# Optimization experiments

Hardware: AMD Instinct MI355X
Metric: run time of the kernel (lower is better)

The kernel has to match this reference:

```python
import jax, jax.numpy as jnp
import numpy as np

NUM_CLASSES = 5
TOPK = 10
ALPHA = 0.5
BETA = 6.0
TEMPERATURE = 2.0
EPS = 1e-9
RADIUS = 1.5
MAXF = 5  # max fallback anchors per tiny GT


def setup_inputs() -> dict:
    key = jax.random.key(0)
    ks = jax.random.split(key, 6)
    B, A, G, C = 16, 8400, 128, NUM_CLASSES
    pred_scores = jax.random.normal(ks[0], (B, A, C), jnp.float32)
    pred_bboxes = jax.random.uniform(ks[1], (B, A, 5), jnp.float32)
    anchor_points = jax.random.uniform(ks[2], (A, 2), jnp.float32)
    gt_labels = jax.random.randint(ks[3], (B, G, 1), 0, C, jnp.int32)
    gt_bboxes = jax.random.uniform(ks[4], (B, G, 5), jnp.float32)
    mask_gt = jax.random.randint(ks[5], (B, G, 1), 0, 2, jnp.int32)
    return dict(pred_scores=pred_scores, pred_bboxes=pred_bboxes,
                anchor_points=anchor_points, gt_labels=gt_labels,
                gt_bboxes=gt_bboxes, mask_gt=mask_gt)


def reference(pred_scores, pred_bboxes, anchor_points, gt_labels, gt_bboxes, mask_gt):
    B, A, C = pred_scores.shape
    G = gt_bboxes.shape[1]
    labels = gt_labels[..., 0].astype(jnp.int32)          # [B,G]
    mask = mask_gt[..., 0] > 0                            # [B,G]

    # ---- get_box_metrics ----
    cls_scores = jnp.clip(jax.nn.sigmoid(pred_scores), EPS, 1.0)            # [B,A,C]
    bbox_scores = jnp.take_along_axis(
        cls_scores, jnp.broadcast_to(labels[:, None, :], (B, A, G)), axis=2)  # [B,A,G]
    pred_cxcy = pred_bboxes[:, :, None, :2]                                  # [B,A,1,2]
    gt_cxcy = gt_bboxes[:, None, :, :2]                                      # [B,1,G,2]
    distances = jnp.linalg.norm(pred_cxcy - gt_cxcy, axis=-1)                # [B,A,G]
    gt_wh = gt_bboxes[:, None, :, 2:4]                                       # [B,1,G,2]
    scale = jnp.sqrt(gt_wh[..., 0] * gt_wh[..., 1])                          # [B,1,G]
    overlaps = jnp.exp(-(distances / (scale + 1e-6)) ** 2)                   # [B,A,G]
    align_metric = jnp.exp(ALPHA * jnp.log(bbox_scores + EPS)
                           + BETA * jnp.log(overlaps + EPS))
    ap = anchor_points.reshape(1, A, 1, 2)
    center_dist = jnp.linalg.norm(ap - gt_cxcy, axis=-1)                     # [B,A,G]
    center_weight = jnp.exp(-(center_dist / (scale * 1.5 + 1e-6)) ** 2)
    align_metric = align_metric * center_weight

    # ---- select_candidates_in_gts (rotated boxes) ----
    theta = gt_bboxes[:, None, :, 4]                                         # [B,1,G]
    dx = ap[..., 0] - gt_cxcy[..., 0]
    dy = ap[..., 1] - gt_cxcy[..., 1]
    cos_t, sin_t = jnp.cos(-theta), jnp.sin(-theta)
    local_dx = dx * cos_t - dy * sin_t
    local_dy = dx * sin_t + dy * cos_t
    is_in = ((jnp.abs(local_dx) < gt_wh[..., 0] * RADIUS)
             & (jnp.abs(local_dy) < gt_wh[..., 1] * RADIUS))                 # [B,A,G]

    # ---- tiny-object fallback (unconditional, gated by tiny_missed mask;
    #      equivalent to torch's data-dependent `if` branch) ----
    gt_area = gt_bboxes[..., 2] * gt_bboxes[..., 3]                          # [B,G]
    cand_per_gt = is_in.sum(axis=1)                                          # [B,G]
    tiny_missed = mask & (gt_area < 0.01) & (cand_per_gt == 0)
    fallback_k = jnp.where(gt_area < 0.002, 5, 3)                            # [B,G]
    dist_ga = jnp.linalg.norm(
        gt_bboxes[:, :, None, :2] - anchor_points[None, None, :, :], axis=-1)  # [B,G,A]
    _, closest_idx = jax.lax.top_k(-dist_ga, MAXF)                           # [B,G,5]
    seq = jnp.arange(MAXF)[None, None, :]
    valid_fb = tiny_missed[:, :, None] & (seq < fallback_k[:, :, None])      # [B,G,5]
    b_grid = jnp.arange(B)[:, None, None]
    g_grid = jnp.arange(G)[None, :, None]
    fb = jnp.zeros((B, A, G), jnp.int32).at[b_grid, closest_idx, g_grid].max(
        valid_fb.astype(jnp.int32))
    is_in = is_in | (fb > 0)

    align_metric = align_metric * is_in.astype(align_metric.dtype)

    # ---- select_topk_candidates ----
    am_gT = jnp.swapaxes(align_metric, 1, 2) * mask[:, :, None].astype(align_metric.dtype)  # [B,G,A]
    ov_gT = jnp.swapaxes(overlaps, 1, 2)                                     # [B,G,A]
    topk_metrics, topk_idxs = jax.lax.top_k(am_gT, TOPK)                     # [B,G,K]
    topk_overlaps = jnp.take_along_axis(ov_gT, topk_idxs, axis=2)
    dynamic_k = jnp.clip(jnp.round(topk_overlaps.sum(-1)), 1.0, float(TOPK)) # [B,G]
    k_mask = jnp.arange(TOPK)[None, None, :] < dynamic_k[:, :, None]
    pos_vals = (topk_metrics > EPS) & k_mask
    is_pos_gT = jnp.zeros((B, G, A), bool).at[b_grid, g_grid, topk_idxs].set(pos_vals)

    align_metric = jnp.swapaxes(am_gT, 1, 2)                                 # [B,A,G] (GT-masked)
    is_pos = jnp.swapaxes(is_pos_gT, 1, 2)                                   # [B,A,G]
    anchor_to_gt = jnp.argmax(align_metric, axis=-1)                         # [B,A]
    is_pos_mask = is_pos.sum(-1) > 0                                         # [B,A]
    target_labels = jnp.take_along_axis(labels, anchor_to_gt, axis=1)        # [B,A]
    target_bboxes = jnp.take_along_axis(
        gt_bboxes, jnp.broadcast_to(anchor_to_gt[:, :, None], (B, A, 5)), axis=1)  # [B,A,5]
    am_max = align_metric.max(axis=1, keepdims=True)                         # [B,1,G]
    norm_am = align_metric / (am_max + EPS) * overlaps                       # [B,A,G]
    raw = jnp.take_along_axis(norm_am, anchor_to_gt[:, :, None], axis=2)[..., 0]  # [B,A]
    valid = (target_labels >= 0) & (target_labels < C) & is_pos_mask
    raw_safe = jnp.where(raw > 0, raw, 1.0)
    soft = jnp.where(raw > 0, raw_safe ** (1.0 / TEMPERATURE), 0.0)
    target_scores = jax.nn.one_hot(target_labels, C, dtype=pred_scores.dtype) \
        * (soft * valid.astype(soft.dtype))[..., None]                       # [B,A,C]
    return target_labels, target_bboxes, target_scores, is_pos_mask
```

## Files before the change

### kernel.cpp

```cpp
#include <hip/hip_runtime.h>
#include <math.h>

#define NB 16
#define NA 8400
#define NG 128
#define NC 5
#define KTOP 10
#define MAXF 5


__global__ __launch_bounds__(256) void k_logsig(
    const float* __restrict__ pred_scores, double* __restrict__ table, int n)
{
    int i = blockIdx.x * 256 + threadIdx.x;
    if (i < n) {
        double x = (double)pred_scores[i];
        double s = 1.0 / (1.0 + exp(-x));
        s = fmin(fmax(s, 1e-9), 1.0);
        table[i] = log(s + 1e-9);
    }
}


__global__ __launch_bounds__(256) void k_assign(
    const float* __restrict__ pred_bboxes,
    const float* __restrict__ anchor_points,
    const int*   __restrict__ gt_labels,
    const float* __restrict__ gt_bboxes,
    const int*   __restrict__ mask_gt,
    const double* __restrict__ logsig,
    int* __restrict__ fb_cnt,
    int* __restrict__ fb_idx,
    double* __restrict__ am_max,
    int* __restrict__ pos_mask)
{
    int bg = blockIdx.x;
    int b = bg / NG;
    int tid = threadIdx.x;

    const float* gbb = gt_bboxes + (size_t)bg * 5;
    double cx = gbb[0], cy = gbb[1], w = gbb[2], h = gbb[3], th = gbb[4];
    double ct = cos(-th), st = sin(-th);
    int m = mask_gt[bg];
    double area = (double)gbb[2] * (double)gbb[3];

    __shared__ double Sv[KTOP][256];
    __shared__ int    Si[KTOP][256];
    __shared__ double rv[256];
    __shared__ int    ri[256];
    __shared__ double wv_s[KTOP];
    __shared__ int    wi_s[KTOP];
    __shared__ int    s_icnt[256];
    __shared__ int    s_win[MAXF];
    __shared__ int    s_k;

    bool need_fb = (m > 0) && (area < 0.01);
    if (tid == 0) s_k = 0;
    if (need_fb) {
        int cnt = 0;
        double ld[MAXF]; int li[MAXF];
#pragma unroll
        for (int t = 0; t < MAXF; t++) { ld[t] = 1e300; li[t] = 0x7fffffff; }
        for (int a = tid; a < NA; a += 256) {
            double ax = anchor_points[a * 2], ay = anchor_points[a * 2 + 1];
            double cdx = ax - cx, cdy = ay - cy;
            double ldx = cdx * ct - cdy * st;
            double ldy = cdx * st + cdy * ct;
            if (fabs(ldx) < w * 1.5 && fabs(ldy) < h * 1.5) cnt++;
            double d = sqrt(cdx * cdx + cdy * cdy);
            double cv = d; int ci = a;
#pragma unroll
            for (int p = 0; p < MAXF; p++) {
                bool better = (cv < ld[p]) || (cv == ld[p] && ci < li[p]);
                double tv = ld[p]; int ti = li[p];
                if (better) { ld[p] = cv; li[p] = ci; cv = tv; ci = ti; }
            }
        }
        s_icnt[tid] = cnt;
#pragma unroll
        for (int t = 0; t < MAXF; t++) { Sv[t][tid] = ld[t]; Si[t][tid] = li[t]; }
        __syncthreads();
        for (int s2 = 128; s2 > 0; s2 >>= 1) {
            if (tid < s2) s_icnt[tid] += s_icnt[tid + s2];
            __syncthreads();
        }
        int ptr = 0;
        for (int j = 0; j < MAXF; j++) {
            double hv = (ptr < MAXF) ? Sv[ptr][tid] : 1e300;
            int    hi = (ptr < MAXF) ? Si[ptr][tid] : 0x7fffffff;
            rv[tid] = hv; ri[tid] = hi;
            __syncthreads();
            for (int s2 = 128; s2 > 0; s2 >>= 1) {
                if (tid < s2) {
                    bool better = (rv[tid + s2] < rv[tid]) ||
                                  (rv[tid + s2] == rv[tid] && ri[tid + s2] < ri[tid]);
                    if (better) { rv[tid] = rv[tid + s2]; ri[tid] = ri[tid + s2]; }
                }
                __syncthreads();
            }
            int Wi = ri[0];
            if (tid == 0) s_win[j] = Wi;
            __syncthreads();
            if (ptr < MAXF && hi == Wi) ptr++;
        }
        if (tid == 0) {
            int total = s_icnt[0];
            int k = 0;
            if (total == 0) k = (area < 0.002) ? 5 : 3;
            s_k = k;
            for (int j = 0; j < MAXF; j++) fb_idx[bg * MAXF + j] = s_win[j];
        }
        __syncthreads();
    }
    if (tid == 0) fb_cnt[bg] = s_k;

    if (m <= 0) {
        if (tid == 0) am_max[bg] = 0.0;
        return;
    }
    __syncthreads();

    double scale = sqrt(w * h);
    int lbl = gt_labels[bg];
    int fcnt = s_k;
    int fidx[MAXF];
#pragma unroll
    for (int t = 0; t < MAXF; t++) fidx[t] = need_fb ? s_win[t] : 0x7fffffff;

    double lv[KTOP]; int li2[KTOP];
#pragma unroll
    for (int t = 0; t < KTOP; t++) { lv[t] = -1.0; li2[t] = 0x7fffffff; }

    for (int a = tid; a < NA; a += 256) {
        double ax = anchor_points[a * 2], ay = anchor_points[a * 2 + 1];
        double cdx = ax - cx, cdy = ay - cy;
        double ldx = cdx * ct - cdy * st;
        double ldy = cdx * st + cdy * ct;
        bool inb = (fabs(ldx) < w * 1.5) && (fabs(ldy) < h * 1.5);
        bool fb = false;
#pragma unroll
        for (int t = 0; t < MAXF; t++) if (t < fcnt && fidx[t] == a) fb = true;
        double amm = 0.0;
        if (inb || fb) {
            double lgs = logsig[((size_t)b * NA + a) * NC + lbl];
            double px = pred_bboxes[((size_t)b * NA + a) * 5 + 0];
            double py = pred_bboxes[((size_t)b * NA + a) * 5 + 1];
            double dx = px - cx, dy = py - cy;
            double d  = sqrt(dx * dx + dy * dy);
            double r  = d / (scale + 1e-6);
            double e1 = exp(-(r * r));
            double L  = log(e1 + 1e-9);
            double cd = sqrt(cdx * cdx + cdy * cdy);
            double cr = cd / (scale * 1.5 + 1e-6);
            amm = exp(0.5 * lgs + 6.0 * L - cr * cr);
        }
        double cv = amm; int ci = a;
#pragma unroll
        for (int p = 0; p < KTOP; p++) {
            bool better = (cv > lv[p]) || (cv == lv[p] && ci < li2[p]);
            double tv = lv[p]; int ti = li2[p];
            if (better) { lv[p] = cv; li2[p] = ci; cv = tv; ci = ti; }
        }
    }

#pragma unroll
    for (int t = 0; t < KTOP; t++) { Sv[t][tid] = lv[t]; Si[t][tid] = li2[t]; }
    __syncthreads();

    int ptr = 0;
    for (int j = 0; j < KTOP; j++) {
        double hv = (ptr < KTOP) ? Sv[ptr][tid] : -1.0;
        int    hi = (ptr < KTOP) ? Si[ptr][tid] : 0x7fffffff;
        rv[tid] = hv; ri[tid] = hi;
        __syncthreads();
        for (int s2 = 128; s2 > 0; s2 >>= 1) {
            if (tid < s2) {
                bool better = (rv[tid + s2] > rv[tid]) ||
                              (rv[tid + s2] == rv[tid] && ri[tid + s2] < ri[tid]);
                if (better) { rv[tid] = rv[tid + s2]; ri[tid] = ri[tid + s2]; }
            }
            __syncthreads();
        }
        int Wi = ri[0];
        if (tid == 0) { wv_s[j] = rv[0]; wi_s[j] = Wi; }
        __syncthreads();
        if (ptr < KTOP && hi == Wi) ptr++;
    }

    if (tid == 0) {
        am_max[bg] = wv_s[0];
        double ssum = 0.0;
        for (int j = 0; j < KTOP; j++) {
            int aW = wi_s[j];
            double px = pred_bboxes[((size_t)b * NA + aW) * 5 + 0];
            double py = pred_bboxes[((size_t)b * NA + aW) * 5 + 1];
            double dx = px - cx, dy = py - cy;
            double d = sqrt(dx * dx + dy * dy);
            double r = d / (scale + 1e-6);
            ssum += exp(-(r * r));
        }
        double rk = rint(ssum);
        rk = fmin(fmax(rk, 1.0), 10.0);
        for (int j = 0; j < KTOP; j++) {
            if (wv_s[j] > 1e-9 && (double)j < rk)
                atomicOr(&pos_mask[b * NA + wi_s[j]], 1);
        }
    }
}


__global__ __launch_bounds__(256) void k_final(
    const float* __restrict__ pred_bboxes,
    const float* __restrict__ anchor_points,
    const int*   __restrict__ gt_labels,
    const float* __restrict__ gt_bboxes,
    const int*   __restrict__ mask_gt,
    const double* __restrict__ logsig,
    const int*   __restrict__ fb_cnt,
    const int*   __restrict__ fb_idx,
    const double* __restrict__ am_max,
    const int*   __restrict__ pos_mask,
    float* __restrict__ out)
{
    __shared__ double s_cx[NG], s_cy[NG], s_ct[NG], s_st[NG], s_scale[NG], s_w[NG], s_h[NG], s_am[NG];
    __shared__ int s_lbl[NG], s_msk[NG], s_fcnt[NG];
    __shared__ int s_fidx[NG][MAXF];
    __shared__ double mv[4][64];
    __shared__ int    mg[4][64];
    __shared__ double mo[4][64];

    int b = blockIdx.y;
    int tid = threadIdx.x;
    if (tid < NG) {
        int g = tid, bg = b * NG + g;
        const float* gbb = gt_bboxes + (size_t)bg * 5;
        double th = gbb[4];
        s_cx[g] = gbb[0]; s_cy[g] = gbb[1]; s_w[g] = gbb[2]; s_h[g] = gbb[3];
        s_ct[g] = cos(-th); s_st[g] = sin(-th);
        s_scale[g] = sqrt((double)gbb[2] * (double)gbb[3]);
        s_am[g] = am_max[bg];
        s_lbl[g] = gt_labels[bg];
        s_msk[g] = mask_gt[bg];
        s_fcnt[g] = fb_cnt[bg];
        for (int t = 0; t < MAXF; t++) s_fidx[g][t] = fb_idx[bg * MAXF + t];
    }
    __syncthreads();

    int al = tid & 63;
    int slice = tid >> 6;
    int a = blockIdx.x * 64 + al;

    double best = -1.0; int bestg = slice * 32; double bov = 0.0;
    if (a < NA) {
        double px = pred_bboxes[((size_t)b * NA + a) * 5 + 0];
        double py = pred_bboxes[((size_t)b * NA + a) * 5 + 1];
        double ax = anchor_points[a * 2], ay = anchor_points[a * 2 + 1];
        const double* lg = logsig + ((size_t)b * NA + a) * NC;
        double l0 = lg[0], l1 = lg[1], l2 = lg[2], l3 = lg[3], l4 = lg[4];

        int g0 = slice * 32;
        for (int g = g0; g < g0 + 32; g++) {
            int lbl = s_lbl[g];
            double lgs = (lbl == 0) ? l0 : (lbl == 1) ? l1 : (lbl == 2) ? l2 : (lbl == 3) ? l3 : l4;
            bool fb = false;
            int fc = s_fcnt[g];
#pragma unroll
            for (int t = 0; t < MAXF; t++) if (t < fc && s_fidx[g][t] == a) fb = true;
            double cdx = ax - s_cx[g], cdy = ay - s_cy[g];
            double ldx = cdx * s_ct[g] - cdy * s_st[g];
            double ldy = cdx * s_st[g] + cdy * s_ct[g];
            bool inb = (fabs(ldx) < s_w[g] * 1.5) && (fabs(ldy) < s_h[g] * 1.5);
            double amm = 0.0, e1 = 0.0;
            if ((inb || fb) && s_msk[g] > 0) {
                double dx = px - s_cx[g], dy = py - s_cy[g];
                double d = sqrt(dx * dx + dy * dy);
                double r = d / (s_scale[g] + 1e-6);
                e1 = exp(-(r * r));
                double L = log(e1 + 1e-9);
                double cd = sqrt(cdx * cdx + cdy * cdy);
                double cr = cd / (s_scale[g] * 1.5 + 1e-6);
                amm = exp(0.5 * lgs + 6.0 * L - cr * cr);
            }
            if (amm > best) { best = amm; bestg = g; bov = e1; }
        }
    }

    mv[slice][al] = best; mg[slice][al] = bestg; mo[slice][al] = bov;
    __syncthreads();

    if (tid < 64) {
        int a2 = blockIdx.x * 64 + tid;
        if (a2 < NA) {
            double B = mv[0][tid]; int G = mg[0][tid]; double OV = mo[0][tid];
#pragma unroll
            for (int s = 1; s < 4; s++) {
                if (mv[s][tid] > B) { B = mv[s][tid]; G = mg[s][tid]; OV = mo[s][tid]; }
            }
            int lbl = s_lbl[G];
            bool pos = pos_mask[b * NA + a2] != 0;
            bool valid = (lbl >= 0 && lbl < NC) && pos;
            double raw = B / (s_am[G] + 1e-9) * OV;
            double soft = (raw > 0.0) ? sqrt(raw) : 0.0;

            size_t ba = (size_t)b * NA + a2;
            out[ba] = (float)lbl;
            const float* gb2 = gt_bboxes + ((size_t)b * NG + G) * 5;
            float* ob = out + (size_t)NB * NA + ba * 5;
            ob[0] = gb2[0]; ob[1] = gb2[1]; ob[2] = gb2[2]; ob[3] = gb2[3]; ob[4] = gb2[4];
            float* os = out + (size_t)NB * NA * 6 + ba * 5;
            float sval = valid ? (float)soft : 0.0f;
#pragma unroll
            for (int c = 0; c < NC; c++) os[c] = (c == lbl) ? sval : 0.0f;
            out[(size_t)NB * NA * 11 + ba] = pos ? 1.0f : 0.0f;
        }
    }
}


extern "C" void kernel_launch(void* const* d_in, const int* in_sizes, int n_in,
                              void* d_out, int out_size, void* d_ws, size_t ws_size,
                              hipStream_t stream)
{
    const float* pred_scores   = (const float*)d_in[0];
    const float* pred_bboxes   = (const float*)d_in[1];
    const float* anchor_points = (const float*)d_in[2];
    const int*   gt_labels     = (const int*)d_in[3];
    const float* gt_bboxes     = (const float*)d_in[4];
    const int*   mask_gt       = (const int*)d_in[5];
    float* out = (float*)d_out;

    char* ws = (char*)d_ws;
    size_t off = 0;
    int* pos_mask = (int*)(ws + off);
    off += (size_t)NB * NA * sizeof(int);
    off = (off + 255) & ~(size_t)255;
    double* amax = (double*)(ws + off);
    off += (size_t)NB * NG * sizeof(double);
    off = (off + 255) & ~(size_t)255;
    int* fb_cnt = (int*)(ws + off);
    off += (size_t)NB * NG * sizeof(int);
    off = (off + 255) & ~(size_t)255;
    int* fb_idx = (int*)(ws + off);
    off += (size_t)NB * NG * MAXF * sizeof(int);
    off = (off + 255) & ~(size_t)255;
    double* logsig = (double*)(ws + off);

    hipMemsetAsync(pos_mask, 0, (size_t)NB * NA * sizeof(int), stream);

    int nls = NB * NA * NC;
    k_logsig<<<(nls + 255) / 256, 256, 0, stream>>>(pred_scores, logsig, nls);
    k_assign<<<NB * NG, 256, 0, stream>>>(pred_bboxes, anchor_points, gt_labels,
                                          gt_bboxes, mask_gt, logsig,
                                          fb_cnt, fb_idx, amax, pos_mask);
    k_final<<<dim3((NA + 63) / 64, NB), 256, 0, stream>>>(
        pred_bboxes, anchor_points, gt_labels, gt_bboxes, mask_gt, logsig,
        fb_cnt, fb_idx, amax, pos_mask, out);
}
```

Baseline: 337.2 us.

## Add float upper-bound pruning before fp64 metric, wavefront top-k merges, fuse memset

Replaces the fp64 log-sigmoid table with a float table and adds a cheap float upper bound on the alignment metric. In both k_assign and k_final, the exact double-precision computation runs only when that bound could beat the current threshold: a shared atomicMax bar in k_assign, the running best in k_final. The block-wide shared-memory top-k reductions become wavefront shuffle reductions followed by a 4-way serial merge, and zeroing pos_mask is folded into the prep kernel instead of a separate memset. The safety margin on the float bound has to cover the fast-math error so results stay exact, and the extra branching adds divergence.

```diff
diff --git a/kernel.cpp b/kernel.cpp
--- a/kernel.cpp
+++ b/kernel.cpp
@@ -8,27 +8,35 @@
 #define KTOP 10
 #define MAXF 5
 
-
-__global__ __launch_bounds__(256) void k_logsig(
-    const float* __restrict__ pred_scores, double* __restrict__ table, int n)
+static __device__ __forceinline__ double lgs64_of(float x) {
+    double s = 1.0 / (1.0 + exp(-(double)x));
+    s = fmin(fmax(s, 1e-9), 1.0);
+    return log(s + 1e-9);
+}
+
+
+__global__ __launch_bounds__(256) void k_prep(
+    const float* __restrict__ ps, float* __restrict__ tab, int* __restrict__ pos_mask)
 {
     int i = blockIdx.x * 256 + threadIdx.x;
-    if (i < n) {
-        double x = (double)pred_scores[i];
-        double s = 1.0 / (1.0 + exp(-x));
-        s = fmin(fmax(s, 1e-9), 1.0);
-        table[i] = log(s + 1e-9);
-    }
+    if (i < NB * NA * NC) {
+        float x = ps[i];
+        float s = 1.0f / (1.0f + __expf(-x));
+        s = fminf(fmaxf(s, 1e-9f), 1.0f);
+        tab[i] = __logf(s + 1e-9f);
+    }
+    if (i < NB * NA) pos_mask[i] = 0;
 }
 
 
 __global__ __launch_bounds__(256) void k_assign(
+    const float* __restrict__ pred_scores,
     const float* __restrict__ pred_bboxes,
     const float* __restrict__ anchor_points,
     const int*   __restrict__ gt_labels,
     const float* __restrict__ gt_bboxes,
     const int*   __restrict__ mask_gt,
-    const double* __restrict__ logsig,
+    const float* __restrict__ lg32,
     int* __restrict__ fb_cnt,
     int* __restrict__ fb_idx,
     double* __restrict__ am_max,
@@ -37,74 +45,82 @@
     int bg = blockIdx.x;
     int b = bg / NG;
     int tid = threadIdx.x;
+    int lane = tid & 63;
+    int wid = tid >> 6;
 
     const float* gbb = gt_bboxes + (size_t)bg * 5;
-    double cx = gbb[0], cy = gbb[1], w = gbb[2], h = gbb[3], th = gbb[4];
+    float cxf = gbb[0], cyf = gbb[1];
+    double cx = cxf, cy = cyf, w = gbb[2], h = gbb[3], th = gbb[4];
     double ct = cos(-th), st = sin(-th);
+    double w15 = w * 1.5, h15 = h * 1.5;
     int m = mask_gt[bg];
-    double area = (double)gbb[2] * (double)gbb[3];
-
-    __shared__ double Sv[KTOP][256];
-    __shared__ int    Si[KTOP][256];
-    __shared__ double rv[256];
-    __shared__ int    ri[256];
+    double area = w * h;
+
+    __shared__ unsigned s_bar_u;
+    __shared__ double LwV[4][KTOP];
+    __shared__ int    LwI[4][KTOP];
     __shared__ double wv_s[KTOP];
     __shared__ int    wi_s[KTOP];
-    __shared__ int    s_icnt[256];
     __shared__ int    s_win[MAXF];
     __shared__ int    s_k;
+    __shared__ int    s_cnt;
 
     bool need_fb = (m > 0) && (area < 0.01);
-    if (tid == 0) s_k = 0;
+    if (tid == 0) { s_k = 0; s_cnt = 0; s_bar_u = 0u; }
+    __syncthreads();
+
     if (need_fb) {
         int cnt = 0;
-        double ld[MAXF]; int li[MAXF];
-#pragma unroll
-        for (int t = 0; t < MAXF; t++) { ld[t] = 1e300; li[t] = 0x7fffffff; }
+        double ld[MAXF]; int lid[MAXF];
+#pragma unroll
+        for (int t = 0; t < MAXF; t++) { ld[t] = 1e300; lid[t] = 0x7fffffff; }
         for (int a = tid; a < NA; a += 256) {
-            double ax = anchor_points[a * 2], ay = anchor_points[a * 2 + 1];
-            double cdx = ax - cx, cdy = ay - cy;
+            float axf = anchor_points[2 * a], ayf = anchor_points[2 * a + 1];
+            double cdx = (double)axf - cx, cdy = (double)ayf - cy;
             double ldx = cdx * ct - cdy * st;
             double ldy = cdx * st + cdy * ct;
-            if (fabs(ldx) < w * 1.5 && fabs(ldy) < h * 1.5) cnt++;
+            if (fabs(ldx) < w15 && fabs(ldy) < h15) cnt++;
             double d = sqrt(cdx * cdx + cdy * cdy);
             double cv = d; int ci = a;
 #pragma unroll
             for (int p = 0; p < MAXF; p++) {
-                bool better = (cv < ld[p]) || (cv == ld[p] && ci < li[p]);
-                double tv = ld[p]; int ti = li[p];
-                if (better) { ld[p] = cv; li[p] = ci; cv = tv; ci = ti; }
-            }
-        }
-        s_icnt[tid] = cnt;
-#pragma unroll
-        for (int t = 0; t < MAXF; t++) { Sv[t][tid] = ld[t]; Si[t][tid] = li[t]; }
+                bool better = (cv < ld[p]) || (cv == ld[p] && ci < lid[p]);
+                double tv = ld[p]; int ti = lid[p];
+                if (better) { ld[p] = cv; lid[p] = ci; cv = tv; ci = ti; }
+            }
+        }
+        for (int off = 32; off; off >>= 1) cnt += __shfl_xor(cnt, off);
+        if (lane == 0) atomicAdd(&s_cnt, cnt);
+        for (int j = 0; j < MAXF; j++) {
+            double bv = ld[0]; int bi = lid[0];
+            int hi = lid[0];
+            for (int off = 32; off; off >>= 1) {
+                double ov = __shfl_xor(bv, off); int oi = __shfl_xor(bi, off);
+                if (ov < bv || (ov == bv && oi < bi)) { bv = ov; bi = oi; }
+            }
+            if (lane == 0) { LwV[wid][j] = bv; LwI[wid][j] = bi; }
+            if (hi == bi) {
+#pragma unroll
+                for (int p = 0; p < MAXF - 1; p++) { ld[p] = ld[p + 1]; lid[p] = lid[p + 1]; }
+                ld[MAXF - 1] = 1e301; lid[MAXF - 1] = 0x7fffffff;
+            }
+        }
         __syncthreads();
-        for (int s2 = 128; s2 > 0; s2 >>= 1) {
-            if (tid < s2) s_icnt[tid] += s_icnt[tid + s2];
-            __syncthreads();
-        }
-        int ptr = 0;
-        for (int j = 0; j < MAXF; j++) {
-            double hv = (ptr < MAXF) ? Sv[ptr][tid] : 1e300;
-            int    hi = (ptr < MAXF) ? Si[ptr][tid] : 0x7fffffff;
-            rv[tid] = hv; ri[tid] = hi;
-            __syncthreads();
-            for (int s2 = 128; s2 > 0; s2 >>= 1) {
-                if (tid < s2) {
-                    bool better = (rv[tid + s2] < rv[tid]) ||
-                                  (rv[tid + s2] == rv[tid] && ri[tid + s2] < ri[tid]);
-                    if (better) { rv[tid] = rv[tid + s2]; ri[tid] = ri[tid + s2]; }
-                }
-                __syncthreads();
-            }
-            int Wi = ri[0];
-            if (tid == 0) s_win[j] = Wi;
-            __syncthreads();
-            if (ptr < MAXF && hi == Wi) ptr++;
-        }
         if (tid == 0) {
-            int total = s_icnt[0];
+            int p0 = 0, p1 = 0, p2 = 0, p3 = 0;
+            for (int j = 0; j < MAXF; j++) {
+                double h0 = (p0 < MAXF) ? LwV[0][p0] : 1e302; int i0 = (p0 < MAXF) ? LwI[0][p0] : 0x7fffffff;
+                double h1 = (p1 < MAXF) ? LwV[1][p1] : 1e302; int i1 = (p1 < MAXF) ? LwI[1][p1] : 0x7fffffff;
+                double h2 = (p2 < MAXF) ? LwV[2][p2] : 1e302; int i2 = (p2 < MAXF) ? LwI[2][p2] : 0x7fffffff;
+                double h3 = (p3 < MAXF) ? LwV[3][p3] : 1e302; int i3 = (p3 < MAXF) ? LwI[3][p3] : 0x7fffffff;
+                double bv = h0; int bi = i0; int bw = 0;
+                if (h1 < bv || (h1 == bv && i1 < bi)) { bv = h1; bi = i1; bw = 1; }
+                if (h2 < bv || (h2 == bv && i2 < bi)) { bv = h2; bi = i2; bw = 2; }
+                if (h3 < bv || (h3 == bv && i3 < bi)) { bv = h3; bi = i3; bw = 3; }
+                s_win[j] = bi;
+                if (bw == 0) p0++; else if (bw == 1) p1++; else if (bw == 2) p2++; else p3++;
+            }
+            int total = s_cnt;
             int k = 0;
             if (total == 0) k = (area < 0.002) ? 5 : 3;
             s_k = k;
@@ -121,79 +137,112 @@
     __syncthreads();
 
     double scale = sqrt(w * h);
+    float scalef = (float)scale;
+    float sef = scalef + 1e-6f;
+    float se2f = scalef * 1.5f + 1e-6f;
     int lbl = gt_labels[bg];
     int fcnt = s_k;
     int fidx[MAXF];
 #pragma unroll
     for (int t = 0; t < MAXF; t++) fidx[t] = need_fb ? s_win[t] : 0x7fffffff;
 
-    double lv[KTOP]; int li2[KTOP];
-#pragma unroll
-    for (int t = 0; t < KTOP; t++) { lv[t] = -1.0; li2[t] = 0x7fffffff; }
+    double lv[KTOP]; int li[KTOP];
+#pragma unroll
+    for (int t = 0; t < KTOP; t++) { lv[t] = -1.0; li[t] = 0x7fffffff; }
 
     for (int a = tid; a < NA; a += 256) {
-        double ax = anchor_points[a * 2], ay = anchor_points[a * 2 + 1];
-        double cdx = ax - cx, cdy = ay - cy;
+        float axf = anchor_points[2 * a], ayf = anchor_points[2 * a + 1];
+        double cdx = (double)axf - cx, cdy = (double)ayf - cy;
         double ldx = cdx * ct - cdy * st;
         double ldy = cdx * st + cdy * ct;
-        bool inb = (fabs(ldx) < w * 1.5) && (fabs(ldy) < h * 1.5);
-        bool fb = false;
-#pragma unroll
-        for (int t = 0; t < MAXF; t++) if (t < fcnt && fidx[t] == a) fb = true;
-        double amm = 0.0;
-        if (inb || fb) {
-            double lgs = logsig[((size_t)b * NA + a) * NC + lbl];
-            double px = pred_bboxes[((size_t)b * NA + a) * 5 + 0];
-            double py = pred_bboxes[((size_t)b * NA + a) * 5 + 1];
-            double dx = px - cx, dy = py - cy;
-            double d  = sqrt(dx * dx + dy * dy);
-            double r  = d / (scale + 1e-6);
-            double e1 = exp(-(r * r));
-            double L  = log(e1 + 1e-9);
-            double cd = sqrt(cdx * cdx + cdy * cdy);
-            double cr = cd / (scale * 1.5 + 1e-6);
-            amm = exp(0.5 * lgs + 6.0 * L - cr * cr);
-        }
-        double cv = amm; int ci = a;
-#pragma unroll
-        for (int p = 0; p < KTOP; p++) {
-            bool better = (cv > lv[p]) || (cv == lv[p] && ci < li2[p]);
-            double tv = lv[p]; int ti = li2[p];
-            if (better) { lv[p] = cv; li2[p] = ci; cv = tv; ci = ti; }
-        }
-    }
-
-#pragma unroll
-    for (int t = 0; t < KTOP; t++) { Sv[t][tid] = lv[t]; Si[t][tid] = li2[t]; }
+        bool inb = (fabs(ldx) < w15) && (fabs(ldy) < h15);
+        bool fbh = false;
+#pragma unroll
+        for (int t = 0; t < MAXF; t++) if (t < fcnt && fidx[t] == a) fbh = true;
+        double amm = 0.0; bool have = false;
+        if (inb || fbh) {
+            float pxf = pred_bboxes[((size_t)b * NA + a) * 5 + 0];
+            float pyf = pred_bboxes[((size_t)b * NA + a) * 5 + 1];
+            float lgsf = lg32[((size_t)b * NA + a) * NC + lbl];
+            float dxf = pxf - cxf, dyf = pyf - cyf;
+            float rf = sqrtf(dxf * dxf + dyf * dyf) / sef;
+            float e1f = __expf(-(rf * rf));
+            float Lf = __logf(e1f + 1e-9f);
+            float cdxf = axf - cxf, cdyf = ayf - cyf;
+            float crf = sqrtf(cdxf * cdxf + cdyf * cdyf) / se2f;
+            float t1 = 0.5f * lgsf, t2 = 6.0f * Lf, t3 = crf * crf;
+            float t32 = t1 + t2 - t3;
+            float mm = 2e-4f + 2e-5f * (fabsf(t1) + fabsf(t2) + t3);
+            float ub = __expf(t32 + mm);
+            float barf = __uint_as_float(*(volatile unsigned*)&s_bar_u);
+            if (!(ub < barf)) {
+                double lgs = lgs64_of(pred_scores[((size_t)b * NA + a) * NC + lbl]);
+                double px = (double)pxf, py = (double)pyf;
+                double dx = px - cx, dy = py - cy;
+                double d  = sqrt(dx * dx + dy * dy);
+                double r  = d / (scale + 1e-6);
+                double e1 = exp(-(r * r));
+                double L  = log(e1 + 1e-9);
+                double cd = sqrt(cdx * cdx + cdy * cdy);
+                double cr = cd / (scale * 1.5 + 1e-6);
+                amm = exp(0.5 * lgs + 6.0 * L - cr * cr);
+                have = true;
+            }
+        } else {
+            float barf = __uint_as_float(*(volatile unsigned*)&s_bar_u);
+            if (barf == 0.0f) { amm = 0.0; have = true; }
+        }
+        if (have) {
+            double cv = amm; int ci = a;
+#pragma unroll
+            for (int p = 0; p < KTOP; p++) {
+                bool better = (cv > lv[p]) || (cv == lv[p] && ci < li[p]);
+                double tv = lv[p]; int ti = li[p];
+                if (better) { lv[p] = cv; li[p] = ci; cv = tv; ci = ti; }
+            }
+            if (lv[KTOP - 1] > 0.0) {
+                unsigned nb = __float_as_uint(__double2float_rd(lv[KTOP - 1]));
+                atomicMax(&s_bar_u, nb);
+            }
+        }
+    }
+
+    for (int j = 0; j < KTOP; j++) {
+        double bv = lv[0]; int bi = li[0];
+        int hi = li[0];
+        for (int off = 32; off; off >>= 1) {
+            double ov = __shfl_xor(bv, off); int oi = __shfl_xor(bi, off);
+            if (ov > bv || (ov == bv && oi < bi)) { bv = ov; bi = oi; }
+        }
+        if (lane == 0) { LwV[wid][j] = bv; LwI[wid][j] = bi; }
+        if (hi == bi) {
+#pragma unroll
+            for (int p = 0; p < KTOP - 1; p++) { lv[p] = lv[p + 1]; li[p] = li[p + 1]; }
+            lv[KTOP - 1] = -2.0; li[KTOP - 1] = 0x7fffffff;
+        }
+    }
     __syncthreads();
 
-    int ptr = 0;
-    for (int j = 0; j < KTOP; j++) {
-        double hv = (ptr < KTOP) ? Sv[ptr][tid] : -1.0;
-        int    hi = (ptr < KTOP) ? Si[ptr][tid] : 0x7fffffff;
-        rv[tid] = hv; ri[tid] = hi;
-        __syncthreads();
-        for (int s2 = 128; s2 > 0; s2 >>= 1) {
-            if (tid < s2) {
-                bool better = (rv[tid + s2] > rv[tid]) ||
-                              (rv[tid + s2] == rv[tid] && ri[tid + s2] < ri[tid]);
-                if (better) { rv[tid] = rv[tid + s2]; ri[tid] = ri[tid + s2]; }
-            }
-            __syncthreads();
-        }
-        int Wi = ri[0];
-        if (tid == 0) { wv_s[j] = rv[0]; wi_s[j] = Wi; }
-        __syncthreads();
-        if (ptr < KTOP && hi == Wi) ptr++;
-    }
-
     if (tid == 0) {
+        int p0 = 0, p1 = 0, p2 = 0, p3 = 0;
+        for (int j = 0; j < KTOP; j++) {
+            double h0 = (p0 < KTOP) ? LwV[0][p0] : -3.0; int i0 = (p0 < KTOP) ? LwI[0][p0] : 0x7fffffff;
+            double h1 = (p1 < KTOP) ? LwV[1][p1] : -3.0; int i1 = (p1 < KTOP) ? LwI[1][p1] : 0x7fffffff;
+            double h2 = (p2 < KTOP) ? LwV[2][p2] : -3.0; int i2 = (p2 < KTOP) ? LwI[2][p2] : 0x7fffffff;
+            double h3 = (p3 < KTOP) ? LwV[3][p3] : -3.0; int i3 = (p3 < KTOP) ? LwI[3][p3] : 0x7fffffff;
+            double bv = h0; int bi = i0; int bw = 0;
+            if (h1 > bv || (h1 == bv && i1 < bi)) { bv = h1; bi = i1; bw = 1; }
+            if (h2 > bv || (h2 == bv && i2 < bi)) { bv = h2; bi = i2; bw = 2; }
+            if (h3 > bv || (h3 == bv && i3 < bi)) { bv = h3; bi = i3; bw = 3; }
+            wv_s[j] = bv; wi_s[j] = bi;
+            if (bw == 0) p0++; else if (bw == 1) p1++; else if (bw == 2) p2++; else p3++;
+        }
         am_max[bg] = wv_s[0];
         double ssum = 0.0;
         for (int j = 0; j < KTOP; j++) {
             int aW = wi_s[j];
-            double px = pred_bboxes[((size_t)b * NA + aW) * 5 + 0];
-            double py = pred_bboxes[((size_t)b * NA + aW) * 5 + 1];
+            double px = (double)pred_bboxes[((size_t)b * NA + aW) * 5 + 0];
+            double py = (double)pred_bboxes[((size_t)b * NA + aW) * 5 + 1];
             double dx = px - cx, dy = py - cy;
             double d = sqrt(dx * dx + dy * dy);
             double r = d / (scale + 1e-6);
@@ -210,19 +259,21 @@
 
 
 __global__ __launch_bounds__(256) void k_final(
+    const float* __restrict__ pred_scores,
     const float* __restrict__ pred_bboxes,
     const float* __restrict__ anchor_points,
     const int*   __restrict__ gt_labels,
     const float* __restrict__ gt_bboxes,
     const int*   __restrict__ mask_gt,
-    const double* __restrict__ logsig,
+    const float* __restrict__ lg32,
     const int*   __restrict__ fb_cnt,
     const int*   __restrict__ fb_idx,
     const double* __restrict__ am_max,
     const int*   __restrict__ pos_mask,
     float* __restrict__ out)
 {
-    __shared__ double s_cx[NG], s_cy[NG], s_ct[NG], s_st[NG], s_scale[NG], s_w[NG], s_h[NG], s_am[NG];
+    __shared__ double s_cx[NG], s_cy[NG], s_ct[NG], s_st[NG], s_scale[NG], s_w15[NG], s_h15[NG], s_am[NG];
+    __shared__ float  f_cx[NG], f_cy[NG], f_se[NG], f_se2[NG];
     __shared__ int s_lbl[NG], s_msk[NG], s_fcnt[NG];
     __shared__ int s_fidx[NG][MAXF];
     __shared__ double mv[4][64];
@@ -232,17 +283,23 @@
     int b = blockIdx.y;
     int tid = threadIdx.x;
     if (tid < NG) {
-        int g = tid, bg = b * NG + g;
-        const float* gbb = gt_bboxes + (size_t)bg * 5;
+        int g = tid, bgi = b * NG + g;
+        const float* gbb = gt_bboxes + (size_t)bgi * 5;
         double th = gbb[4];
-        s_cx[g] = gbb[0]; s_cy[g] = gbb[1]; s_w[g] = gbb[2]; s_h[g] = gbb[3];
+        double w = gbb[2], h = gbb[3];
+        s_cx[g] = gbb[0]; s_cy[g] = gbb[1];
+        s_w15[g] = w * 1.5; s_h15[g] = h * 1.5;
         s_ct[g] = cos(-th); s_st[g] = sin(-th);
-        s_scale[g] = sqrt((double)gbb[2] * (double)gbb[3]);
-        s_am[g] = am_max[bg];
-        s_lbl[g] = gt_labels[bg];
-        s_msk[g] = mask_gt[bg];
-        s_fcnt[g] = fb_cnt[bg];
-        for (int t = 0; t < MAXF; t++) s_fidx[g][t] = fb_idx[bg * MAXF + t];
+        double sc = sqrt(w * h);
+        s_scale[g] = sc;
+        f_cx[g] = gbb[0]; f_cy[g] = gbb[1];
+        float scf = (float)sc;
+        f_se[g] = scf + 1e-6f; f_se2[g] = scf * 1.5f + 1e-6f;
+        s_am[g] = am_max[bgi];
+        s_lbl[g] = gt_labels[bgi];
+        s_msk[g] = mask_gt[bgi];
+        s_fcnt[g] = fb_cnt[bgi];
+        for (int t = 0; t < MAXF; t++) s_fidx[g][t] = fb_idx[bgi * MAXF + t];
     }
     __syncthreads();
 
@@ -252,26 +309,40 @@
 
     double best = -1.0; int bestg = slice * 32; double bov = 0.0;
     if (a < NA) {
-        double px = pred_bboxes[((size_t)b * NA + a) * 5 + 0];
-        double py = pred_bboxes[((size_t)b * NA + a) * 5 + 1];
-        double ax = anchor_points[a * 2], ay = anchor_points[a * 2 + 1];
-        const double* lg = logsig + ((size_t)b * NA + a) * NC;
-        double l0 = lg[0], l1 = lg[1], l2 = lg[2], l3 = lg[3], l4 = lg[4];
+        float pxf = pred_bboxes[((size_t)b * NA + a) * 5 + 0];
+        float pyf = pred_bboxes[((size_t)b * NA + a) * 5 + 1];
+        float axf = anchor_points[2 * a], ayf = anchor_points[2 * a + 1];
+        const float* lg = lg32 + ((size_t)b * NA + a) * NC;
+        float l0 = lg[0], l1 = lg[1], l2 = lg[2], l3 = lg[3], l4 = lg[4];
+        double px = pxf, py = pyf;
+        float bestf = -1.0f;
 
         int g0 = slice * 32;
         for (int g = g0; g < g0 + 32; g++) {
-            int lbl = s_lbl[g];
-            double lgs = (lbl == 0) ? l0 : (lbl == 1) ? l1 : (lbl == 2) ? l2 : (lbl == 3) ? l3 : l4;
-            bool fb = false;
-            int fc = s_fcnt[g];
-#pragma unroll
-            for (int t = 0; t < MAXF; t++) if (t < fc && s_fidx[g][t] == a) fb = true;
-            double cdx = ax - s_cx[g], cdy = ay - s_cy[g];
+            double cdx = (double)axf - s_cx[g], cdy = (double)ayf - s_cy[g];
             double ldx = cdx * s_ct[g] - cdy * s_st[g];
             double ldy = cdx * s_st[g] + cdy * s_ct[g];
-            bool inb = (fabs(ldx) < s_w[g] * 1.5) && (fabs(ldy) < s_h[g] * 1.5);
+            bool inb = (fabs(ldx) < s_w15[g]) && (fabs(ldy) < s_h15[g]);
+            bool fbh = false;
+            int fc = s_fcnt[g];
+#pragma unroll
+            for (int t = 0; t < MAXF; t++) if (t < fc && s_fidx[g][t] == a) fbh = true;
             double amm = 0.0, e1 = 0.0;
-            if ((inb || fb) && s_msk[g] > 0) {
+            if ((inb || fbh) && s_msk[g] > 0) {
+                int lbl = s_lbl[g];
+                float lgsf = (lbl == 0) ? l0 : (lbl == 1) ? l1 : (lbl == 2) ? l2 : (lbl == 3) ? l3 : l4;
+                float dxf = pxf - f_cx[g], dyf = pyf - f_cy[g];
+                float rf = sqrtf(dxf * dxf + dyf * dyf) / f_se[g];
+                float e1f = __expf(-(rf * rf));
+                float Lf = __logf(e1f + 1e-9f);
+                float cdxf = axf - f_cx[g], cdyf = ayf - f_cy[g];
+                float crf = sqrtf(cdxf * cdxf + cdyf * cdyf) / f_se2[g];
+                float t1 = 0.5f * lgsf, t2 = 6.0f * Lf, t3 = crf * crf;
+                float t32 = t1 + t2 - t3;
+                float mm = 2e-4f + 2e-5f * (fabsf(t1) + fabsf(t2) + t3);
+                float ub = __expf(t32 + mm);
+                if (ub < bestf) continue;
+                double lgs = lgs64_of(pred_scores[((size_t)b * NA + a) * NC + lbl]);
                 double dx = px - s_cx[g], dy = py - s_cy[g];
                 double d = sqrt(dx * dx + dy * dy);
                 double r = d / (s_scale[g] + 1e-6);
@@ -281,7 +352,10 @@
                 double cr = cd / (s_scale[g] * 1.5 + 1e-6);
                 amm = exp(0.5 * lgs + 6.0 * L - cr * cr);
             }
-            if (amm > best) { best = amm; bestg = g; bov = e1; }
+            if (amm > best) {
+                best = amm; bestg = g; bov = e1;
+                bestf = __double2float_rd(best);
+            }
         }
     }
 
@@ -343,16 +417,14 @@
     int* fb_idx = (int*)(ws + off);
     off += (size_t)NB * NG * MAXF * sizeof(int);
     off = (off + 255) & ~(size_t)255;
-    double* logsig = (double*)(ws + off);
-
-    hipMemsetAsync(pos_mask, 0, (size_t)NB * NA * sizeof(int), stream);
+    float* lg32 = (float*)(ws + off);
 
     int nls = NB * NA * NC;
-    k_logsig<<<(nls + 255) / 256, 256, 0, stream>>>(pred_scores, logsig, nls);
-    k_assign<<<NB * NG, 256, 0, stream>>>(pred_bboxes, anchor_points, gt_labels,
-                                          gt_bboxes, mask_gt, logsig,
+    k_prep<<<(nls + 255) / 256, 256, 0, stream>>>(pred_scores, lg32, pos_mask);
+    k_assign<<<NB * NG, 256, 0, stream>>>(pred_scores, pred_bboxes, anchor_points, gt_labels,
+                                          gt_bboxes, mask_gt, lg32,
                                           fb_cnt, fb_idx, amax, pos_mask);
     k_final<<<dim3((NA + 63) / 64, NB), 256, 0, stream>>>(
-        pred_bboxes, anchor_points, gt_labels, gt_bboxes, mask_gt, logsig,
+        pred_scores, pred_bboxes, anchor_points, gt_labels, gt_bboxes, mask_gt, lg32,
         fb_cnt, fb_idx, amax, pos_mask, out);
 }
```

Result: slower. 431.4 us (+27.9%).
